# Optimization experiments

Hardware: AMD Instinct MI355X
Metric: run time of the kernel (lower is better)

## Reference

```python
import jax, jax.numpy as jnp
import numpy as np

STEPS = 3
TOP_N = 2
ROUTE_TEMP = 1.5


def setup_inputs() -> dict:
    key = jax.random.key(0)
    ks = jax.random.split(key, 7)
    B, H, W, C = 16, 112, 112, 128
    heads, dh = 2, 64
    hd = heads * dh  # 128
    K = 4
    s_in = 0.02  # keep activations well-scaled through 3 steps
    x = jax.random.normal(ks[0], (B, H, W, C), dtype=jnp.float32)
    Wk = jax.random.normal(ks[1], (C, hd), dtype=jnp.float32) * s_in
    Wv = jax.random.normal(ks[2], (C, hd), dtype=jnp.float32) * s_in
    q = jax.random.normal(ks[3], (heads, dh), dtype=jnp.float32) * 0.1
    Wmlp = jax.random.normal(ks[4], (hd, K), dtype=jnp.float32) * 0.1
    Wb = jax.random.normal(ks[5], (K, C, C), dtype=jnp.float32) * (1.0 / np.sqrt(C))
    alpha = jnp.zeros((), dtype=jnp.float32)  # attn_log_alpha
    return {"x": x, "Wk": Wk, "Wv": Wv, "q": q, "Wmlp": Wmlp, "Wb": Wb, "alpha": alpha}


def _router(x, Wk, Wv, q, Wmlp):
    # AttnPoolRouter: 1x1 conv K/V, single-query-per-head softmax attention pool.
    B, H, W, C = x.shape
    heads, dh = q.shape
    L = H * W
    k = jnp.einsum('bhwc,ce->bhwe', x, Wk).reshape(B, L, heads, dh)  # [B,L,h,d]
    v = jnp.einsum('bhwc,ce->bhwe', x, Wv).reshape(B, L, heads, dh)
    scores = jnp.einsum('hd,blhd->bhl', q, k) / jnp.sqrt(jnp.asarray(dh, x.dtype))
    attn = jax.nn.softmax(scores, axis=-1)                            # [B,h,L]
    pooled = jnp.einsum('bhl,blhd->bhd', attn, v).reshape(B, heads * dh)
    logits = pooled @ Wmlp                                            # [B,K]
    attn_map = attn.mean(axis=1).reshape(B, H, W, 1)                  # [B,H,W,1]
    return logits, attn_map


def reference(x, Wk, Wv, q, Wmlp, Wb, alpha):
    B, H, W, C = x.shape
    K = Wmlp.shape[1]
    scale = jnp.asarray(H * W, x.dtype)
    a = jax.nn.softplus(alpha)
    for _ in range(STEPS):
        logits, attn_map = _router(x, Wk, Wv, q, Wmlp)
        weights = jax.nn.softmax(logits / ROUTE_TEMP, axis=-1)        # [B,K]
        _, top_idx = jax.lax.top_k(weights, TOP_N)                    # [B,top_n]
        top_mask = jax.nn.one_hot(top_idx, K, dtype=weights.dtype).sum(axis=1)
        wm = weights * top_mask
        ws = wm / (wm.sum(axis=-1, keepdims=True) + 1e-9)
        # straight-through: forward = renormalized top-n, gradient flows to full softmax
        wst = ws + jax.lax.stop_gradient(weights - ws)                # [B,K]
        x_mod = x * (1.0 + attn_map * scale * a)                      # [B,H,W,C]
        # all K branch 1x1 convs, combined by straight-through weights
        x = jnp.einsum('bhwc,kcd,bk->bhwd', x_mod, Wb, wst)
    return x
```

## Files before the change

### kernel.cpp

```cpp
#include <hip/hip_runtime.h>
#include <hip/hip_bf16.h>
#include <cstdint>

#define NB 16
#define NC 128
#define NL 12544
#define NHD 128
#define NK 4
#define ROWS (NB*NL)
#define PCH 49
#define CHROWS 256

typedef unsigned short ushort_t;
typedef __attribute__((ext_vector_type(8))) short bf16x8;
typedef __attribute__((ext_vector_type(4))) float f32x4;

__device__ __forceinline__ float bf2f(unsigned int u){
  union { unsigned int i; float f; } v; v.i = u << 16; return v.f;
}
__device__ __forceinline__ ushort_t f2bf(float f){
  __hip_bfloat16 h = __float2bfloat16(f);
  return *reinterpret_cast<ushort_t*>(&h);
}

__global__ void k_prep(const float* __restrict__ Wk, const float* __restrict__ q,
                       const float* __restrict__ alpha, float* __restrict__ qk,
                       float* __restrict__ scale_a){
  int t = threadIdx.x;
  if (t < NC*2){
    int c = t >> 1, h = t & 1;
    float s = 0.f;
    for (int d = 0; d < 64; ++d) s += Wk[c*NHD + h*64 + d] * q[h*64 + d];
    qk[c*2 + h] = s * 0.125f;
  }
  if (t == 0){
    float a = alpha[0];
    float sp = (a > 20.f) ? a : log1pf(expf(a));
    *scale_a = (float)NL * sp;
  }
}

template<typename XT>
__global__ void __launch_bounds__(256,2) k_pass1(const XT* __restrict__ x,
    const float* __restrict__ qk, float* __restrict__ sraw,
    float* __restrict__ pm, float* __restrict__ pS, float* __restrict__ pP){
  __shared__ __align__(16) ushort_t xs[CHROWS*NC];
  __shared__ float sh0[CHROWS], sh1[CHROWS];
  __shared__ float red[8];
  int b = blockIdx.x / PCH, chunk = blockIdx.x % PCH;
  int l0 = chunk*CHROWS;
  int t = threadIdx.x, lane = t & 63, wave = t >> 6;
  int hi = lane >> 4, n16 = lane & 15;

  if constexpr (sizeof(XT) == 4){
    const float* src = (const float*)x + ((size_t)b*NL + l0)*NC;
    #pragma unroll
    for (int i = 0; i < 16; ++i){
      int idx = i*2048 + t*8;
      int row = idx >> 7;
      float4 v0 = *(const float4*)(src + idx);
      float4 v1 = *(const float4*)(src + idx + 4);
      uint4 p;
      p.x = (unsigned)f2bf(v0.x) | ((unsigned)f2bf(v0.y) << 16);
      p.y = (unsigned)f2bf(v0.z) | ((unsigned)f2bf(v0.w) << 16);
      p.z = (unsigned)f2bf(v1.x) | ((unsigned)f2bf(v1.y) << 16);
      p.w = (unsigned)f2bf(v1.z) | ((unsigned)f2bf(v1.w) << 16);
      *(uint4*)((char*)xs + ((idx*2) ^ ((row & 7) << 4))) = p;
    }
  } else {
    const ushort_t* src = (const ushort_t*)x + ((size_t)b*NL + l0)*NC;
    #pragma unroll
    for (int i = 0; i < 16; ++i){
      int idx = i*2048 + t*8;
      int row = idx >> 7;
      uint4 v = *(const uint4*)(src + idx);
      *(uint4*)((char*)xs + ((idx*2) ^ ((row & 7) << 4))) = v;
    }
  }

  bf16x8 qfv[4];
  #pragma unroll
  for (int kk = 0; kk < 4; ++kk)
    #pragma unroll
    for (int j = 0; j < 8; ++j){
      int k = kk*32 + hi*8 + j;
      qfv[kk][j] = (n16 < 2) ? (short)f2bf(qk[k*2 + n16]) : (short)0;
    }
  __syncthreads();

  #pragma unroll
  for (int rt4 = 0; rt4 < 4; ++rt4){
    int rt = wave*4 + rt4;
    f32x4 acc = (f32x4){0.f,0.f,0.f,0.f};
    #pragma unroll
    for (int kk = 0; kk < 4; ++kk){
      int row = rt*16 + n16;
      int k = kk*32 + hi*8;
      bf16x8 a = *(const bf16x8*)((const char*)xs + ((row*256 + k*2) ^ ((row & 7) << 4)));
      acc = __builtin_amdgcn_mfma_f32_16x16x32_bf16(a, qfv[kk], acc, 0, 0, 0);
    }
    if (n16 < 2){
      float* dst = n16 ? sh1 : sh0;
      #pragma unroll
      for (int r = 0; r < 4; ++r) dst[rt*16 + hi*4 + r] = acc[r];
    }
  }
  __syncthreads();

  float s0 = sh0[t], s1 = sh1[t];
  sraw[((size_t)b*2 + 0)*NL + l0 + t] = s0;
  sraw[((size_t)b*2 + 1)*NL + l0 + t] = s1;
  float m0 = s0, m1 = s1;
  #pragma unroll
  for (int m = 32; m; m >>= 1){ m0 = fmaxf(m0, __shfl_xor(m0, m)); m1 = fmaxf(m1, __shfl_xor(m1, m)); }
  if (lane == 0){ red[wave] = m0; red[4+wave] = m1; }
  __syncthreads();
  m0 = fmaxf(fmaxf(red[0], red[1]), fmaxf(red[2], red[3]));
  m1 = fmaxf(fmaxf(red[4], red[5]), fmaxf(red[6], red[7]));
  float e0 = __expf(s0 - m0), e1 = __expf(s1 - m1);
  float t0 = e0, t1 = e1;
  #pragma unroll
  for (int m = 32; m; m >>= 1){ t0 += __shfl_xor(t0, m); t1 += __shfl_xor(t1, m); }
  __syncthreads();
  if (lane == 0){ red[wave] = t0; red[4+wave] = t1; }
  sh0[t] = e0; sh1[t] = e1;
  __syncthreads();
  if (t == 0){
    pm[(b*2+0)*PCH + chunk] = m0;  pm[(b*2+1)*PCH + chunk] = m1;
    pS[(b*2+0)*PCH + chunk] = red[0]+red[1]+red[2]+red[3];
    pS[(b*2+1)*PCH + chunk] = red[4]+red[5]+red[6]+red[7];
  }

  int h = t >> 7, half = (t >> 6) & 1, cp = t & 63;
  const float* es = h ? sh1 : sh0;
  float a0 = 0.f, a1 = 0.f;
  #pragma unroll 4
  for (int i = 0; i < 128; ++i){
    int l = half*128 + i;
    float e = es[l];
    unsigned u = *(const unsigned*)((const char*)xs + ((l*256 + 4*cp) ^ ((l & 7) << 4)));
    a0 += e * bf2f(u & 0xffffu);
    a1 += e * bf2f(u >> 16);
  }
  __syncthreads();
  if (half){ sh0[h*128 + cp*2] = a0; sh0[h*128 + cp*2 + 1] = a1; }
  __syncthreads();
  if (!half){
    a0 += sh0[h*128 + cp*2];
    a1 += sh0[h*128 + cp*2 + 1];
    float2 w; w.x = a0; w.y = a1;
    *(float2*)&pP[(((size_t)b*PCH + chunk)*2 + h)*NC + 2*cp] = w;
  }
}

__global__ void k_combine(const float* __restrict__ pm, const float* __restrict__ pS,
    const float* __restrict__ pP, const float* __restrict__ Wv,
    const float* __restrict__ Wmlp, const float* __restrict__ Wb,
    ushort_t* __restrict__ WT, float* __restrict__ amS){
  int b = blockIdx.x, t = threadIdx.x;
  __shared__ float w49[2][PCH];
  __shared__ float pxs[2][NC];
  __shared__ float vpool[NHD];
  __shared__ float wts[NK];
  __shared__ float mS[4];
  if (t < 2){
    float m = -3.4e38f;
    for (int j = 0; j < PCH; ++j) m = fmaxf(m, pm[(b*2+t)*PCH + j]);
    float S = 0.f;
    for (int j = 0; j < PCH; ++j) S += pS[(b*2+t)*PCH + j] * __expf(pm[(b*2+t)*PCH + j] - m);
    float iS = 1.f/S;
    mS[t] = m; mS[2+t] = iS;
    amS[(b*2+t)*2 + 0] = m; amS[(b*2+t)*2 + 1] = iS;
  }
  __syncthreads();
  if (t < 2*PCH){ int h = t/PCH, j = t%PCH; w49[h][j] = __expf(pm[(b*2+h)*PCH + j] - mS[h]); }
  __syncthreads();
  {
    int h = t >> 7, c = t & 127;
    float s = 0.f;
    for (int j = 0; j < PCH; ++j) s += pP[(((size_t)b*PCH + j)*2 + h)*NC + c] * w49[h][j];
    pxs[h][c] = s * mS[2+h];
  }
  __syncthreads();
  if (t < NHD){
    int h = t >> 6, d = t & 63;
    float s = 0.f;
    for (int c = 0; c < NC; ++c) s += pxs[h][c] * Wv[c*NHD + h*64 + d];
    vpool[t] = s;
  }
  __syncthreads();
  if (t < NK){
    float s = 0.f;
    for (int e = 0; e < NHD; ++e) s += vpool[e] * Wmlp[e*NK + t];
    wts[t] = s * (1.0f/1.5f);
  }
  __syncthreads();
  if (t == 0){
    float m = fmaxf(fmaxf(wts[0], wts[1]), fmaxf(wts[2], wts[3]));
    float e0 = __expf(wts[0]-m), e1 = __expf(wts[1]-m), e2 = __expf(wts[2]-m), e3 = __expf(wts[3]-m);
    float inv = 1.f/(e0+e1+e2+e3);
    wts[0] = e0*inv; wts[1] = e1*inv; wts[2] = e2*inv; wts[3] = e3*inv;
  }
  __syncthreads();
  float w0 = wts[0], w1 = wts[1], w2 = wts[2], w3 = wts[3];
  for (int idx = t; idx < NC*NHD; idx += 256){
    int d = idx >> 7, c = idx & 127;
    const float* wb = Wb + (size_t)c*NC + d;
    float v = w0*wb[0] + w1*wb[NC*NC] + w2*wb[2*NC*NC] + w3*wb[3*NC*NC];
    WT[(size_t)b*NC*NHD + d*NC + c] = f2bf(v);
  }
}

template<typename XIN, typename XOUT>
__global__ void __launch_bounds__(256,2) k_gemm(const XIN* __restrict__ xin,
    const ushort_t* __restrict__ WT, const float* __restrict__ sraw,
    const float* __restrict__ amS, const float* __restrict__ scale_a,
    XOUT* __restrict__ xout){
  __shared__ __align__(16) ushort_t lA[128*128];
  __shared__ __align__(16) ushort_t lB[128*128];
  const int nchunk = NL/128;
  int b = blockIdx.x / nchunk, chunk = blockIdx.x % nchunk;
  int l0 = chunk*128;
  int t = threadIdx.x;
  float sa = scale_a[0]*0.5f;
  float am0 = amS[(b*2+0)*2+0], ai0 = amS[(b*2+0)*2+1];
  float am1 = amS[(b*2+1)*2+0], ai1 = amS[(b*2+1)*2+1];
  const float* s0p = sraw + ((size_t)b*2 + 0)*NL + l0;
  const float* s1p = sraw + ((size_t)b*2 + 1)*NL + l0;

  {
    const ushort_t* src = WT + (size_t)b*NC*NHD;
    #pragma unroll
    for (int i = 0; i < 8; ++i){
      int idx = i*2048 + t*8;
      int d = idx >> 7, c = idx & 127;
      uint4 v = *(const uint4*)(src + idx);
      int byo = (d*256 + c*2) ^ ((d & 7) << 4);
      *(uint4*)((char*)lB + byo) = v;
    }
  }
  if constexpr (sizeof(XIN) == 4){
    const float* src = (const float*)xin + ((size_t)b*NL + l0)*NC;
    #pragma unroll
    for (int i = 0; i < 16; ++i){
      int idx = i*1024 + t*4;
      int row = idx >> 7, c = idx & 127;
      float4 v = *(const float4*)(src + idx);
      float mod = 1.f + sa*(__expf(s0p[row]-am0)*ai0 + __expf(s1p[row]-am1)*ai1);
      unsigned int p0 = (unsigned)f2bf(v.x*mod) | ((unsigned)f2bf(v.y*mod) << 16);
      unsigned int p1 = (unsigned)f2bf(v.z*mod) | ((unsigned)f2bf(v.w*mod) << 16);
      int byo = (row*256 + c*2) ^ ((row & 7) << 4);
      *(uint2*)((char*)lA + byo) = make_uint2(p0, p1);
    }
  } else {
    const ushort_t* src = (const ushort_t*)xin + ((size_t)b*NL + l0)*NC;
    #pragma unroll
    for (int i = 0; i < 8; ++i){
      int idx = i*2048 + t*8;
      int row = idx >> 7, c = idx & 127;
      uint4 v = *(const uint4*)(src + idx);
      float mod = 1.f + sa*(__expf(s0p[row]-am0)*ai0 + __expf(s1p[row]-am1)*ai1);
      unsigned int vv[4] = {v.x, v.y, v.z, v.w};
      unsigned int r[4];
      #pragma unroll
      for (int j = 0; j < 4; ++j){
        float lo = bf2f(vv[j] & 0xffffu)*mod, hi2 = bf2f(vv[j] >> 16)*mod;
        r[j] = (unsigned)f2bf(lo) | ((unsigned)f2bf(hi2) << 16);
      }
      int byo = (row*256 + c*2) ^ ((row & 7) << 4);
      *(uint4*)((char*)lA + byo) = make_uint4(r[0], r[1], r[2], r[3]);
    }
  }
  __syncthreads();

  int lane = t & 63, wave = t >> 6;
  int trow = lane & 15, kg = lane >> 4;
  int r0 = wave*32;
  f32x4 acc[2][8];
  #pragma unroll
  for (int m = 0; m < 2; ++m)
    #pragma unroll
    for (int n = 0; n < 8; ++n) acc[m][n] = (f32x4){0.f,0.f,0.f,0.f};

  #pragma unroll
  for (int kk = 0; kk < 4; ++kk){
    int k = kk*32 + kg*8;
    int ra0 = r0 + trow, ra1 = r0 + 16 + trow;
    bf16x8 a0 = *(const bf16x8*)((const char*)lA + ((ra0*256 + k*2) ^ ((ra0 & 7) << 4)));
    bf16x8 a1 = *(const bf16x8*)((const char*)lA + ((ra1*256 + k*2) ^ ((ra1 & 7) << 4)));
    #pragma unroll
    for (int nt = 0; nt < 8; ++nt){
      int col = nt*16 + trow;
      bf16x8 bf = *(const bf16x8*)((const char*)lB + ((col*256 + k*2) ^ ((col & 7) << 4)));
      acc[0][nt] = __builtin_amdgcn_mfma_f32_16x16x32_bf16(a0, bf, acc[0][nt], 0, 0, 0);
      acc[1][nt] = __builtin_amdgcn_mfma_f32_16x16x32_bf16(a1, bf, acc[1][nt], 0, 0, 0);
    }
  }

  size_t base = ((size_t)b*NL + l0)*NC;
  #pragma unroll
  for (int m = 0; m < 2; ++m)
    #pragma unroll
    for (int nt = 0; nt < 8; ++nt)
      #pragma unroll
      for (int r = 0; r < 4; ++r){
        int row = r0 + m*16 + kg*4 + r;
        int col = nt*16 + trow;
        float v = acc[m][nt][r];
        if constexpr (sizeof(XOUT) == 4) ((float*)xout)[base + (size_t)row*NC + col] = v;
        else                             ((ushort_t*)xout)[base + (size_t)row*NC + col] = f2bf(v);
      }
}

extern "C" void kernel_launch(void* const* d_in, const int* in_sizes, int n_in,
                              void* d_out, int out_size, void* d_ws, size_t ws_size,
                              hipStream_t stream){
  const float* x0   = (const float*)d_in[0];
  const float* Wk   = (const float*)d_in[1];
  const float* Wv   = (const float*)d_in[2];
  const float* q    = (const float*)d_in[3];
  const float* Wmlp = (const float*)d_in[4];
  const float* Wb   = (const float*)d_in[5];
  const float* alpha= (const float*)d_in[6];
  float* out = (float*)d_out;

  char* ws = (char*)d_ws;
  float* qk      = (float*)ws;
  float* scale_a = qk + 256;
  float* sraw    = qk + 320;
  float* pm      = sraw + (size_t)NB*2*NL;
  float* pS      = pm + NB*2*PCH;
  float* pP      = pS + NB*2*PCH;
  float* amS     = pP + (size_t)NB*PCH*2*NC;
  ushort_t* WT   = (ushort_t*)(amS + NB*4);
  char* endfixed = (char*)(WT + (size_t)NB*NC*NHD);
  size_t xoff    = ((size_t)(endfixed - ws) + 255) & ~(size_t)255;
  ushort_t* xb   = (ushort_t*)(ws + xoff);
  bool big = ws_size >= xoff + (size_t)ROWS*NC*2;

  k_prep<<<1, 256, 0, stream>>>(Wk, q, alpha, qk, scale_a);

  for (int step = 0; step < 3; ++step){
    const void* xi; void* xo; bool xi_bf, xo_bf;
    if (big){
      if (step == 0){ xi = x0;  xi_bf = false; xo = xb;  xo_bf = true;  }
      else if (step == 1){ xi = xb; xi_bf = true; xo = xb; xo_bf = true; }
      else { xi = xb; xi_bf = true; xo = out; xo_bf = false; }
    } else {
      xi = (step == 0) ? (const void*)x0 : (const void*)out;
      xi_bf = false; xo = out; xo_bf = false;
    }

    if (xi_bf) k_pass1<ushort_t><<<NB*PCH, 256, 0, stream>>>((const ushort_t*)xi, qk, sraw, pm, pS, pP);
    else       k_pass1<float   ><<<NB*PCH, 256, 0, stream>>>((const float*)xi, qk, sraw, pm, pS, pP);

    k_combine<<<NB, 256, 0, stream>>>(pm, pS, pP, Wv, Wmlp, Wb, WT, amS);

    dim3 g(NB*(NL/128));
    if (xi_bf){
      if (xo_bf) k_gemm<ushort_t, ushort_t><<<g, 256, 0, stream>>>((const ushort_t*)xi, WT, sraw, amS, scale_a, (ushort_t*)xo);
      else       k_gemm<ushort_t, float   ><<<g, 256, 0, stream>>>((const ushort_t*)xi, WT, sraw, amS, scale_a, (float*)xo);
    } else {
      if (xo_bf) k_gemm<float, ushort_t><<<g, 256, 0, stream>>>((const float*)xi, WT, sraw, amS, scale_a, (ushort_t*)xo);
      else       k_gemm<float, float   ><<<g, 256, 0, stream>>>((const float*)xi, WT, sraw, amS, scale_a, (float*)xo);
    }
  }
}
```

Measured before the change: 453.2 us.

## Fuse next-step router statistics into GEMM epilogue, dropping per-step pass1

The router's attention-pool statistics for the next step (scores, per-chunk max/sum, weighted pooled x) are now computed inside the GEMM epilogue from the fp32 accumulators. Pass1 runs only once, on the original input, so the two later re-reads of the activation tensor go away. Chunk size drops to 128 rows (98 chunks per batch) with a remapped block order. k_combine gains wave-parallel reductions and an LDS transpose for building WT. The cost is a heavier GEMM epilogue with extra shuffles and syncs, and the stats now come from unrounded fp32 outputs rather than the stored bf16 values.

After: 388.1 us. 1.17x faster.

```diff
diff --git a/kernel.cpp b/kernel.cpp
--- a/kernel.cpp
+++ b/kernel.cpp
@@ -8,8 +8,8 @@
 #define NHD 128
 #define NK 4
 #define ROWS (NB*NL)
-#define PCH 49
-#define CHROWS 256
+#define CH 128
+#define PCH2 98
 
 typedef unsigned short ushort_t;
 typedef __attribute__((ext_vector_type(8))) short bf16x8;
@@ -40,44 +40,31 @@
   }
 }
 
-template<typename XT>
-__global__ void __launch_bounds__(256,2) k_pass1(const XT* __restrict__ x,
+__global__ void __launch_bounds__(256,4) k_pass1(const float* __restrict__ x,
     const float* __restrict__ qk, float* __restrict__ sraw,
     float* __restrict__ pm, float* __restrict__ pS, float* __restrict__ pP){
-  __shared__ __align__(16) ushort_t xs[CHROWS*NC];
-  __shared__ float sh0[CHROWS], sh1[CHROWS];
+  __shared__ __align__(16) ushort_t xs[CH*NC];
+  __shared__ float shs0[CH], shs1[CH];
   __shared__ float red[8];
-  int b = blockIdx.x / PCH, chunk = blockIdx.x % PCH;
-  int l0 = chunk*CHROWS;
+  __shared__ float pmerge[256];
+  int wg = ((blockIdx.x & 7) * 196) + (blockIdx.x >> 3);
+  int b = wg / PCH2, chunk = wg % PCH2;
+  int l0 = chunk*CH;
   int t = threadIdx.x, lane = t & 63, wave = t >> 6;
   int hi = lane >> 4, n16 = lane & 15;
 
-  if constexpr (sizeof(XT) == 4){
-    const float* src = (const float*)x + ((size_t)b*NL + l0)*NC;
+  {
+    const float* src = x + ((size_t)b*NL + l0)*NC;
     #pragma unroll
     for (int i = 0; i < 16; ++i){
-      int idx = i*2048 + t*8;
+      int idx = i*1024 + t*4;
       int row = idx >> 7;
-      float4 v0 = *(const float4*)(src + idx);
-      float4 v1 = *(const float4*)(src + idx + 4);
-      uint4 p;
-      p.x = (unsigned)f2bf(v0.x) | ((unsigned)f2bf(v0.y) << 16);
-      p.y = (unsigned)f2bf(v0.z) | ((unsigned)f2bf(v0.w) << 16);
-      p.z = (unsigned)f2bf(v1.x) | ((unsigned)f2bf(v1.y) << 16);
-      p.w = (unsigned)f2bf(v1.z) | ((unsigned)f2bf(v1.w) << 16);
-      *(uint4*)((char*)xs + ((idx*2) ^ ((row & 7) << 4))) = p;
-    }
-  } else {
-    const ushort_t* src = (const ushort_t*)x + ((size_t)b*NL + l0)*NC;
-    #pragma unroll
-    for (int i = 0; i < 16; ++i){
-      int idx = i*2048 + t*8;
-      int row = idx >> 7;
-      uint4 v = *(const uint4*)(src + idx);
-      *(uint4*)((char*)xs + ((idx*2) ^ ((row & 7) << 4))) = v;
-    }
-  }
-
+      float4 v = *(const float4*)(src + idx);
+      unsigned p0 = (unsigned)f2bf(v.x) | ((unsigned)f2bf(v.y) << 16);
+      unsigned p1 = (unsigned)f2bf(v.z) | ((unsigned)f2bf(v.w) << 16);
+      *(uint2*)((char*)xs + ((idx*2) ^ ((row & 7) << 4))) = make_uint2(p0, p1);
+    }
+  }
   bf16x8 qfv[4];
   #pragma unroll
   for (int kk = 0; kk < 4; ++kk)
@@ -89,8 +76,8 @@
   __syncthreads();
 
   #pragma unroll
-  for (int rt4 = 0; rt4 < 4; ++rt4){
-    int rt = wave*4 + rt4;
+  for (int rt2 = 0; rt2 < 2; ++rt2){
+    int rt = wave*2 + rt2;
     f32x4 acc = (f32x4){0.f,0.f,0.f,0.f};
     #pragma unroll
     for (int kk = 0; kk < 4; ++kk){
@@ -100,56 +87,57 @@
       acc = __builtin_amdgcn_mfma_f32_16x16x32_bf16(a, qfv[kk], acc, 0, 0, 0);
     }
     if (n16 < 2){
-      float* dst = n16 ? sh1 : sh0;
+      float* dst = n16 ? shs1 : shs0;
       #pragma unroll
       for (int r = 0; r < 4; ++r) dst[rt*16 + hi*4 + r] = acc[r];
     }
   }
   __syncthreads();
 
-  float s0 = sh0[t], s1 = sh1[t];
-  sraw[((size_t)b*2 + 0)*NL + l0 + t] = s0;
-  sraw[((size_t)b*2 + 1)*NL + l0 + t] = s1;
+  float s0 = -3.4e38f, s1 = -3.4e38f;
+  if (t < 128){
+    s0 = shs0[t]; s1 = shs1[t];
+    sraw[((size_t)b*2+0)*NL + l0 + t] = s0;
+    sraw[((size_t)b*2+1)*NL + l0 + t] = s1;
+  }
   float m0 = s0, m1 = s1;
   #pragma unroll
-  for (int m = 32; m; m >>= 1){ m0 = fmaxf(m0, __shfl_xor(m0, m)); m1 = fmaxf(m1, __shfl_xor(m1, m)); }
-  if (lane == 0){ red[wave] = m0; red[4+wave] = m1; }
-  __syncthreads();
-  m0 = fmaxf(fmaxf(red[0], red[1]), fmaxf(red[2], red[3]));
-  m1 = fmaxf(fmaxf(red[4], red[5]), fmaxf(red[6], red[7]));
-  float e0 = __expf(s0 - m0), e1 = __expf(s1 - m1);
+  for (int mk = 32; mk; mk >>= 1){ m0 = fmaxf(m0, __shfl_xor(m0, mk)); m1 = fmaxf(m1, __shfl_xor(m1, mk)); }
+  if (lane == 0 && wave < 2){ red[wave] = m0; red[2+wave] = m1; }
+  __syncthreads();
+  float M0 = fmaxf(red[0], red[1]), M1 = fmaxf(red[2], red[3]);
+  float e0 = 0.f, e1 = 0.f;
+  if (t < 128){ e0 = __expf(s0 - M0); e1 = __expf(s1 - M1); shs0[t] = e0; shs1[t] = e1; }
   float t0 = e0, t1 = e1;
   #pragma unroll
-  for (int m = 32; m; m >>= 1){ t0 += __shfl_xor(t0, m); t1 += __shfl_xor(t1, m); }
-  __syncthreads();
-  if (lane == 0){ red[wave] = t0; red[4+wave] = t1; }
-  sh0[t] = e0; sh1[t] = e1;
+  for (int mk = 32; mk; mk >>= 1){ t0 += __shfl_xor(t0, mk); t1 += __shfl_xor(t1, mk); }
+  if (lane == 0 && wave < 2){ red[4+wave] = t0; red[6+wave] = t1; }
   __syncthreads();
   if (t == 0){
-    pm[(b*2+0)*PCH + chunk] = m0;  pm[(b*2+1)*PCH + chunk] = m1;
-    pS[(b*2+0)*PCH + chunk] = red[0]+red[1]+red[2]+red[3];
-    pS[(b*2+1)*PCH + chunk] = red[4]+red[5]+red[6]+red[7];
+    pm[(b*2+0)*PCH2 + chunk] = M0; pm[(b*2+1)*PCH2 + chunk] = M1;
+    pS[(b*2+0)*PCH2 + chunk] = red[4]+red[5];
+    pS[(b*2+1)*PCH2 + chunk] = red[6]+red[7];
   }
 
   int h = t >> 7, half = (t >> 6) & 1, cp = t & 63;
-  const float* es = h ? sh1 : sh0;
+  const float* es = h ? shs1 : shs0;
   float a0 = 0.f, a1 = 0.f;
   #pragma unroll 4
-  for (int i = 0; i < 128; ++i){
-    int l = half*128 + i;
+  for (int i = 0; i < 64; ++i){
+    int l = half*64 + i;
     float e = es[l];
     unsigned u = *(const unsigned*)((const char*)xs + ((l*256 + 4*cp) ^ ((l & 7) << 4)));
     a0 += e * bf2f(u & 0xffffu);
     a1 += e * bf2f(u >> 16);
   }
   __syncthreads();
-  if (half){ sh0[h*128 + cp*2] = a0; sh0[h*128 + cp*2 + 1] = a1; }
+  if (half){ pmerge[h*128 + cp*2] = a0; pmerge[h*128 + cp*2 + 1] = a1; }
   __syncthreads();
   if (!half){
-    a0 += sh0[h*128 + cp*2];
-    a1 += sh0[h*128 + cp*2 + 1];
+    a0 += pmerge[h*128 + cp*2];
+    a1 += pmerge[h*128 + cp*2 + 1];
     float2 w; w.x = a0; w.y = a1;
-    *(float2*)&pP[(((size_t)b*PCH + chunk)*2 + h)*NC + 2*cp] = w;
+    *(float2*)&pP[(((size_t)b*PCH2 + chunk)*2 + h)*NC + 2*cp] = w;
   }
 }
 
@@ -157,29 +145,40 @@
     const float* __restrict__ pP, const float* __restrict__ Wv,
     const float* __restrict__ Wmlp, const float* __restrict__ Wb,
     ushort_t* __restrict__ WT, float* __restrict__ amS){
-  int b = blockIdx.x, t = threadIdx.x;
-  __shared__ float w49[2][PCH];
+  int b = blockIdx.x, t = threadIdx.x, lane = t & 63, wave = t >> 6;
+  __shared__ float w98[2][PCH2];
   __shared__ float pxs[2][NC];
   __shared__ float vpool[NHD];
   __shared__ float wts[NK];
-  __shared__ float mS[4];
-  if (t < 2){
+  __shared__ float mSh[4];
+  __shared__ float wcomb[NC*129];
+
+  if (wave < 2){
+    int h = wave;
+    const float* pmh = pm + (b*2+h)*PCH2;
+    const float* pSh = pS + (b*2+h)*PCH2;
     float m = -3.4e38f;
-    for (int j = 0; j < PCH; ++j) m = fmaxf(m, pm[(b*2+t)*PCH + j]);
+    for (int j = lane; j < PCH2; j += 64) m = fmaxf(m, pmh[j]);
+    #pragma unroll
+    for (int mk = 32; mk; mk >>= 1) m = fmaxf(m, __shfl_xor(m, mk));
     float S = 0.f;
-    for (int j = 0; j < PCH; ++j) S += pS[(b*2+t)*PCH + j] * __expf(pm[(b*2+t)*PCH + j] - m);
-    float iS = 1.f/S;
-    mS[t] = m; mS[2+t] = iS;
-    amS[(b*2+t)*2 + 0] = m; amS[(b*2+t)*2 + 1] = iS;
-  }
-  __syncthreads();
-  if (t < 2*PCH){ int h = t/PCH, j = t%PCH; w49[h][j] = __expf(pm[(b*2+h)*PCH + j] - mS[h]); }
+    for (int j = lane; j < PCH2; j += 64) S += pSh[j] * __expf(pmh[j] - m);
+    #pragma unroll
+    for (int mk = 32; mk; mk >>= 1) S += __shfl_xor(S, mk);
+    for (int j = lane; j < PCH2; j += 64) w98[h][j] = __expf(pmh[j] - m);
+    if (lane == 0){
+      float iS = 1.f/S;
+      mSh[h] = m; mSh[2+h] = iS;
+      amS[(b*2+h)*2 + 0] = m; amS[(b*2+h)*2 + 1] = iS;
+    }
+  }
   __syncthreads();
   {
     int h = t >> 7, c = t & 127;
     float s = 0.f;
-    for (int j = 0; j < PCH; ++j) s += pP[(((size_t)b*PCH + j)*2 + h)*NC + c] * w49[h][j];
-    pxs[h][c] = s * mS[2+h];
+    #pragma unroll 2
+    for (int j = 0; j < PCH2; ++j) s += pP[(((size_t)b*PCH2 + j)*2 + h)*NC + c] * w98[h][j];
+    pxs[h][c] = s * mSh[2+h];
   }
   __syncthreads();
   if (t < NHD){
@@ -203,24 +202,33 @@
   }
   __syncthreads();
   float w0 = wts[0], w1 = wts[1], w2 = wts[2], w3 = wts[3];
+  for (int idx = t; idx < NC*NC; idx += 256){
+    int c = idx >> 7, d = idx & 127;
+    const float* wb = Wb + (size_t)c*NC + d;
+    wcomb[c*129 + d] = w0*wb[0] + w1*wb[NC*NC] + w2*wb[2*NC*NC] + w3*wb[3*NC*NC];
+  }
+  __syncthreads();
   for (int idx = t; idx < NC*NHD; idx += 256){
     int d = idx >> 7, c = idx & 127;
-    const float* wb = Wb + (size_t)c*NC + d;
-    float v = w0*wb[0] + w1*wb[NC*NC] + w2*wb[2*NC*NC] + w3*wb[3*NC*NC];
-    WT[(size_t)b*NC*NHD + d*NC + c] = f2bf(v);
-  }
-}
-
-template<typename XIN, typename XOUT>
+    WT[(size_t)b*NC*NHD + d*NC + c] = f2bf(wcomb[c*129 + d]);
+  }
+}
+
+template<typename XIN, typename XOUT, bool STATS>
 __global__ void __launch_bounds__(256,2) k_gemm(const XIN* __restrict__ xin,
-    const ushort_t* __restrict__ WT, const float* __restrict__ sraw,
-    const float* __restrict__ amS, const float* __restrict__ scale_a,
-    XOUT* __restrict__ xout){
-  __shared__ __align__(16) ushort_t lA[128*128];
-  __shared__ __align__(16) ushort_t lB[128*128];
-  const int nchunk = NL/128;
-  int b = blockIdx.x / nchunk, chunk = blockIdx.x % nchunk;
-  int l0 = chunk*128;
+    const ushort_t* __restrict__ WT, const float* __restrict__ qkg,
+    float* __restrict__ sraw, const float* __restrict__ amS,
+    const float* __restrict__ scale_a, XOUT* __restrict__ xout,
+    float* __restrict__ pm, float* __restrict__ pS, float* __restrict__ pP){
+  __shared__ __align__(16) ushort_t lA[CH*NC];
+  __shared__ __align__(16) ushort_t lB[NC*NHD];
+  __shared__ float sqk[256];
+  __shared__ float shs0[CH], shs1[CH];
+  __shared__ float red[8];
+  __shared__ float pacc[4][2][NC];
+  int wg = ((blockIdx.x & 7) * 196) + (blockIdx.x >> 3);
+  int b = wg / PCH2, chunk = wg % PCH2;
+  int l0 = chunk*CH;
   int t = threadIdx.x;
   float sa = scale_a[0]*0.5f;
   float am0 = amS[(b*2+0)*2+0], ai0 = amS[(b*2+0)*2+1];
@@ -228,15 +236,16 @@
   const float* s0p = sraw + ((size_t)b*2 + 0)*NL + l0;
   const float* s1p = sraw + ((size_t)b*2 + 1)*NL + l0;
 
+  if (STATS){ sqk[t] = qkg[t]; }
+
   {
     const ushort_t* src = WT + (size_t)b*NC*NHD;
     #pragma unroll
     for (int i = 0; i < 8; ++i){
       int idx = i*2048 + t*8;
-      int d = idx >> 7, c = idx & 127;
+      int d = idx >> 7;
       uint4 v = *(const uint4*)(src + idx);
-      int byo = (d*256 + c*2) ^ ((d & 7) << 4);
-      *(uint4*)((char*)lB + byo) = v;
+      *(uint4*)((char*)lB + ((idx*2) ^ ((d & 7) << 4))) = v;
     }
   }
   if constexpr (sizeof(XIN) == 4){
@@ -244,31 +253,29 @@
     #pragma unroll
     for (int i = 0; i < 16; ++i){
       int idx = i*1024 + t*4;
-      int row = idx >> 7, c = idx & 127;
+      int row = idx >> 7;
       float4 v = *(const float4*)(src + idx);
       float mod = 1.f + sa*(__expf(s0p[row]-am0)*ai0 + __expf(s1p[row]-am1)*ai1);
-      unsigned int p0 = (unsigned)f2bf(v.x*mod) | ((unsigned)f2bf(v.y*mod) << 16);
-      unsigned int p1 = (unsigned)f2bf(v.z*mod) | ((unsigned)f2bf(v.w*mod) << 16);
-      int byo = (row*256 + c*2) ^ ((row & 7) << 4);
-      *(uint2*)((char*)lA + byo) = make_uint2(p0, p1);
+      unsigned p0 = (unsigned)f2bf(v.x*mod) | ((unsigned)f2bf(v.y*mod) << 16);
+      unsigned p1 = (unsigned)f2bf(v.z*mod) | ((unsigned)f2bf(v.w*mod) << 16);
+      *(uint2*)((char*)lA + ((idx*2) ^ ((row & 7) << 4))) = make_uint2(p0, p1);
     }
   } else {
     const ushort_t* src = (const ushort_t*)xin + ((size_t)b*NL + l0)*NC;
     #pragma unroll
     for (int i = 0; i < 8; ++i){
       int idx = i*2048 + t*8;
-      int row = idx >> 7, c = idx & 127;
+      int row = idx >> 7;
       uint4 v = *(const uint4*)(src + idx);
       float mod = 1.f + sa*(__expf(s0p[row]-am0)*ai0 + __expf(s1p[row]-am1)*ai1);
-      unsigned int vv[4] = {v.x, v.y, v.z, v.w};
-      unsigned int r[4];
+      unsigned vv[4] = {v.x, v.y, v.z, v.w};
+      unsigned r[4];
       #pragma unroll
       for (int j = 0; j < 4; ++j){
         float lo = bf2f(vv[j] & 0xffffu)*mod, hi2 = bf2f(vv[j] >> 16)*mod;
         r[j] = (unsigned)f2bf(lo) | ((unsigned)f2bf(hi2) << 16);
       }
-      int byo = (row*256 + c*2) ^ ((row & 7) << 4);
-      *(uint4*)((char*)lA + byo) = make_uint4(r[0], r[1], r[2], r[3]);
+      *(uint4*)((char*)lA + ((idx*2) ^ ((row & 7) << 4))) = make_uint4(r[0], r[1], r[2], r[3]);
     }
   }
   __syncthreads();
@@ -310,6 +317,87 @@
         if constexpr (sizeof(XOUT) == 4) ((float*)xout)[base + (size_t)row*NC + col] = v;
         else                             ((ushort_t*)xout)[base + (size_t)row*NC + col] = f2bf(v);
       }
+
+  if (STATS){
+    float wq0[8], wq1[8];
+    #pragma unroll
+    for (int nt = 0; nt < 8; ++nt){
+      wq0[nt] = sqk[(nt*16 + trow)*2 + 0];
+      wq1[nt] = sqk[(nt*16 + trow)*2 + 1];
+    }
+    #pragma unroll
+    for (int m = 0; m < 2; ++m)
+      #pragma unroll
+      for (int r = 0; r < 4; ++r){
+        float p0 = 0.f, p1 = 0.f;
+        #pragma unroll
+        for (int nt = 0; nt < 8; ++nt){ float v = acc[m][nt][r]; p0 += v*wq0[nt]; p1 += v*wq1[nt]; }
+        #pragma unroll
+        for (int mk = 1; mk < 16; mk <<= 1){ p0 += __shfl_xor(p0, mk); p1 += __shfl_xor(p1, mk); }
+        int idx = m*4 + r;
+        if (trow == idx){
+          int row = r0 + m*16 + kg*4 + r;
+          shs0[row] = p0; shs1[row] = p1;
+        }
+      }
+    __syncthreads();
+
+    float s0 = -3.4e38f, s1 = -3.4e38f;
+    if (t < 128){
+      s0 = shs0[t]; s1 = shs1[t];
+      sraw[((size_t)b*2+0)*NL + l0 + t] = s0;
+      sraw[((size_t)b*2+1)*NL + l0 + t] = s1;
+    }
+    float m0 = s0, m1 = s1;
+    #pragma unroll
+    for (int mk = 32; mk; mk >>= 1){ m0 = fmaxf(m0, __shfl_xor(m0, mk)); m1 = fmaxf(m1, __shfl_xor(m1, mk)); }
+    if (lane == 0 && wave < 2){ red[wave] = m0; red[2+wave] = m1; }
+    __syncthreads();
+    float M0 = fmaxf(red[0], red[1]), M1 = fmaxf(red[2], red[3]);
+    float e0 = 0.f, e1 = 0.f;
+    if (t < 128){ e0 = __expf(s0 - M0); e1 = __expf(s1 - M1); shs0[t] = e0; shs1[t] = e1; }
+    float t0 = e0, t1 = e1;
+    #pragma unroll
+    for (int mk = 32; mk; mk >>= 1){ t0 += __shfl_xor(t0, mk); t1 += __shfl_xor(t1, mk); }
+    if (lane == 0 && wave < 2){ red[4+wave] = t0; red[6+wave] = t1; }
+    __syncthreads();
+    if (t == 0){
+      pm[(b*2+0)*PCH2 + chunk] = M0; pm[(b*2+1)*PCH2 + chunk] = M1;
+      pS[(b*2+0)*PCH2 + chunk] = red[4]+red[5];
+      pS[(b*2+1)*PCH2 + chunk] = red[6]+red[7];
+    }
+
+    float ea0[2][4], ea1[2][4];
+    #pragma unroll
+    for (int m = 0; m < 2; ++m)
+      #pragma unroll
+      for (int r = 0; r < 4; ++r){
+        int row = r0 + m*16 + kg*4 + r;
+        ea0[m][r] = shs0[row]; ea1[m][r] = shs1[row];
+      }
+    #pragma unroll
+    for (int nt = 0; nt < 8; ++nt){
+      float p0 = 0.f, p1 = 0.f;
+      #pragma unroll
+      for (int m = 0; m < 2; ++m)
+        #pragma unroll
+        for (int r = 0; r < 4; ++r){
+          p0 += ea0[m][r]*acc[m][nt][r];
+          p1 += ea1[m][r]*acc[m][nt][r];
+        }
+      p0 += __shfl_xor(p0, 16); p0 += __shfl_xor(p0, 32);
+      p1 += __shfl_xor(p1, 16); p1 += __shfl_xor(p1, 32);
+      int col = nt*16 + trow;
+      if (kg == 0) pacc[wave][0][col] = p0;
+      if (kg == 1) pacc[wave][1][col] = p1;
+    }
+    __syncthreads();
+    {
+      int h = t >> 7, c = t & 127;
+      pP[(((size_t)b*PCH2 + chunk)*2 + h)*NC + c] =
+        pacc[0][h][c] + pacc[1][h][c] + pacc[2][h][c] + pacc[3][h][c];
+    }
+  }
 }
 
 extern "C" void kernel_launch(void* const* d_in, const int* in_sizes, int n_in,
@@ -329,9 +417,9 @@
   float* scale_a = qk + 256;
   float* sraw    = qk + 320;
   float* pm      = sraw + (size_t)NB*2*NL;
-  float* pS      = pm + NB*2*PCH;
-  float* pP      = pS + NB*2*PCH;
-  float* amS     = pP + (size_t)NB*PCH*2*NC;
+  float* pS      = pm + NB*2*PCH2;
+  float* pP      = pS + NB*2*PCH2;
+  float* amS     = pP + (size_t)NB*PCH2*2*NC;
   ushort_t* WT   = (ushort_t*)(amS + NB*4);
   char* endfixed = (char*)(WT + (size_t)NB*NC*NHD);
   size_t xoff    = ((size_t)(endfixed - ws) + 255) & ~(size_t)255;
@@ -340,29 +428,26 @@
 
   k_prep<<<1, 256, 0, stream>>>(Wk, q, alpha, qk, scale_a);
 
+  k_pass1<<<NB*PCH2, 256, 0, stream>>>(x0, qk, sraw, pm, pS, pP);
+
+  dim3 g(NB*PCH2);
   for (int step = 0; step < 3; ++step){
-    const void* xi; void* xo; bool xi_bf, xo_bf;
+    k_combine<<<NB, 256, 0, stream>>>(pm, pS, pP, Wv, Wmlp, Wb, WT, amS);
+
     if (big){
-      if (step == 0){ xi = x0;  xi_bf = false; xo = xb;  xo_bf = true;  }
-      else if (step == 1){ xi = xb; xi_bf = true; xo = xb; xo_bf = true; }
-      else { xi = xb; xi_bf = true; xo = out; xo_bf = false; }
+      if (step == 0)
+        k_gemm<float, ushort_t, true ><<<g, 256, 0, stream>>>(x0, WT, qk, sraw, amS, scale_a, xb, pm, pS, pP);
+      else if (step == 1)
+        k_gemm<ushort_t, ushort_t, true ><<<g, 256, 0, stream>>>(xb, WT, qk, sraw, amS, scale_a, xb, pm, pS, pP);
+      else
+        k_gemm<ushort_t, float, false><<<g, 256, 0, stream>>>(xb, WT, qk, sraw, amS, scale_a, out, pm, pS, pP);
     } else {
-      xi = (step == 0) ? (const void*)x0 : (const void*)out;
-      xi_bf = false; xo = out; xo_bf = false;
-    }
-
-    if (xi_bf) k_pass1<ushort_t><<<NB*PCH, 256, 0, stream>>>((const ushort_t*)xi, qk, sraw, pm, pS, pP);
-    else       k_pass1<float   ><<<NB*PCH, 256, 0, stream>>>((const float*)xi, qk, sraw, pm, pS, pP);
-
-    k_combine<<<NB, 256, 0, stream>>>(pm, pS, pP, Wv, Wmlp, Wb, WT, amS);
-
-    dim3 g(NB*(NL/128));
-    if (xi_bf){
-      if (xo_bf) k_gemm<ushort_t, ushort_t><<<g, 256, 0, stream>>>((const ushort_t*)xi, WT, sraw, amS, scale_a, (ushort_t*)xo);
-      else       k_gemm<ushort_t, float   ><<<g, 256, 0, stream>>>((const ushort_t*)xi, WT, sraw, amS, scale_a, (float*)xo);
-    } else {
-      if (xo_bf) k_gemm<float, ushort_t><<<g, 256, 0, stream>>>((const float*)xi, WT, sraw, amS, scale_a, (ushort_t*)xo);
-      else       k_gemm<float, float   ><<<g, 256, 0, stream>>>((const float*)xi, WT, sraw, amS, scale_a, (float*)xo);
-    }
-  }
-}
+      if (step == 0)
+        k_gemm<float, float, true ><<<g, 256, 0, stream>>>(x0, WT, qk, sraw, amS, scale_a, out, pm, pS, pP);
+      else if (step == 1)
+        k_gemm<float, float, true ><<<g, 256, 0, stream>>>(out, WT, qk, sraw, amS, scale_a, out, pm, pS, pP);
+      else
+        k_gemm<float, float, false><<<g, 256, 0, stream>>>(out, WT, qk, sraw, amS, scale_a, out, pm, pS, pP);
+    }
+  }
+}
```
